# Optimization experiments

Hardware: AMD Instinct MI355X
Metric: run time of the kernel (lower is better)

## Reference

```python
import jax, jax.numpy as jnp
import numpy as np

NUM_NODES = 120000   # entity count
D = 128              # graph_emb_size
T = 10               # time_steps / train_year
B = 64               # batch of input_ids
R = 4                # num_rel
N = 64               # max neighbors per relation (padded)
C = 64               # TCN channel width (output_size)
I = 64               # influence_emb_size
K = 2                # kernel size
L = 8                # TCN levels (num_channels = [64]*8)


def _causal_conv(x, w, b, d):
    # x: [M, Cin, T], w: [Cout, Cin, k] -> causal dilated conv -> [M, Cout, T]
    pad = (w.shape[-1] - 1) * d
    y = jax.lax.conv_general_dilated(x, w, window_strides=(1,), padding=[(pad, 0)],
                                     rhs_dilation=(d,), dimension_numbers=('NCH', 'OIH', 'NCH'))
    return y + b[None, :, None]


def _tcn_last(x, w1_0, b1_0, w2_0, b2_0, down_w, down_b, w1, b1, w2, b2):
    # Bai-style TemporalConvNet; x: [M, D, T] -> last-step state [M, C]
    y = jax.nn.relu(_causal_conv(x, w1_0, b1_0, 1))
    y = jax.nn.relu(_causal_conv(y, w2_0, b2_0, 1))
    h = jax.nn.relu(y + _causal_conv(x, down_w, down_b, 1))  # 1x1 downsample residual (Cin != C)
    for i in range(1, L):
        d = 2 ** i
        y = jax.nn.relu(_causal_conv(h, w1[i - 1], b1[i - 1], d))
        y = jax.nn.relu(_causal_conv(y, w2[i - 1], b2[i - 1], d))
        h = jax.nn.relu(y + h)
    return h[..., -1]


def setup_inputs() -> dict:
    key = jax.random.key(0)
    ks = jax.random.split(key, 16)
    embeddings = jax.random.normal(ks[0], (T, NUM_NODES, D), jnp.float32)
    # entity -> per-year row index; negative = entity absent that year (zero-padded)
    alignment = jax.random.randint(ks[1], (NUM_NODES, T), -NUM_NODES // 5, NUM_NODES).astype(jnp.int32)
    neighbor_idx = jax.random.randint(ks[2], (B, R, N), 0, NUM_NODES).astype(jnp.int32)
    neighbor_mask = jax.random.randint(ks[3], (B, R, N), 0, 2).astype(bool)
    g = lambda k, sh, s: jax.random.normal(k, sh, jnp.float32) * s
    return {
        'embeddings': embeddings,
        'w1_0': g(ks[4], (R, C, D, K), (2.0 / (D * K)) ** 0.5),
        'b1_0': jnp.zeros((R, C), jnp.float32),
        'w2_0': g(ks[5], (R, C, C, K), (2.0 / (C * K)) ** 0.5),
        'b2_0': jnp.zeros((R, C), jnp.float32),
        'down_w': g(ks[6], (R, C, D, 1), (2.0 / D) ** 0.5),
        'down_b': jnp.zeros((R, C), jnp.float32),
        'w1': g(ks[7], (R, L - 1, C, C, K), (2.0 / (C * K)) ** 0.5),
        'b1': jnp.zeros((R, L - 1, C), jnp.float32),
        'w2': g(ks[8], (R, L - 1, C, C, K), (2.0 / (C * K)) ** 0.5),
        'b2': jnp.zeros((R, L - 1, C), jnp.float32),
        'rel_w': g(ks[9], (R, C, I), (2.0 / (C + I)) ** 0.5),
        'alignment': alignment,
        'neighbor_idx': neighbor_idx,
        'neighbor_mask': neighbor_mask,
    }


def reference(embeddings, w1_0, b1_0, w2_0, b2_0, down_w, down_b, w1, b1, w2, b2,
              rel_w, alignment, neighbor_idx, neighbor_mask):
    seq = alignment[neighbor_idx]                                   # [B,R,N,T]
    valid = (seq >= 0) & neighbor_mask[..., None]                   # per-year + existence mask
    idx = jnp.clip(seq, 0)
    # per-year gather: embeddings[t][idx[...,t]] -> [B,R,N,D,T]
    gath = jax.vmap(lambda e, i: e[i], in_axes=(0, -1), out_axes=-1)(embeddings, idx)
    x = gath * valid[:, :, :, None, :].astype(gath.dtype)           # zero-pad absent years
    x = jnp.transpose(x, (1, 0, 2, 3, 4)).reshape(R, B * N, D, T)   # relation-major, neighbors as batch
    last = jax.vmap(_tcn_last)(x, w1_0, b1_0, w2_0, b2_0, down_w, down_b, w1, b1, w2, b2)  # [R,B*N,C]
    infl = jnp.einsum('rmc,rci->rmi', last, rel_w).reshape(R, B, N, I)
    m = jnp.transpose(neighbor_mask, (1, 0, 2)).astype(infl.dtype)  # [R,B,N] drop padded neighbors
    return jnp.einsum('rbni,rbn->bi', infl, m)                      # sum over neighbors and relations
```

## Files before the change

### kernel.cpp

```cpp
#include <hip/hip_runtime.h>
#include <hip/hip_bf16.h>
#include <stdint.h>

constexpr int NUM_NODES = 120000;
constexpr int Tn = 10;
constexpr int Bb = 64, Rr = 4, Nn = 64, Cc = 64, Ii = 64;
constexpr int G = 8;
constexpr int RSTR  = 147456;
constexpr int OFF0  = 0;
constexpr int OFF1  = 16384;
constexpr int OFF2  = 24576;
constexpr int OFFL0 = 32768;

constexpr int OFF_X  = 0;
constexpr int OFF_H0 = 0;
constexpr int OFF_H1 = 6144;
constexpr int OFF_H2 = 10240;
constexpr int OFF_H3 = 12288;
constexpr int OFF_Y  = 20480;
constexpr int ZOFF   = 30720;
constexpr int SMEMB  = 30976;

typedef __attribute__((ext_vector_type(8))) short bf16x8;
typedef __attribute__((ext_vector_type(4))) float f32x4;
typedef __attribute__((ext_vector_type(4))) short s16x4;

__device__ __forceinline__ short f2bf(float f) {
  __hip_bfloat16 h = __float2bfloat16(f);
  return *reinterpret_cast<short*>(&h);
}
__device__ __forceinline__ float bf2f(short s) {
  union { unsigned int u; float f; } x;
  x.u = ((unsigned int)(unsigned short)s) << 16;
  return x.f;
}

extern "C" __global__ void prep_kernel(const float* __restrict__ w1_0,
                                       const float* __restrict__ w2_0,
                                       const float* __restrict__ down_w,
                                       const float* __restrict__ w1s,
                                       const float* __restrict__ w2s,
                                       short* __restrict__ Wf) {
  int i0 = blockIdx.x * blockDim.x + threadIdx.x;
  int stride = gridDim.x * blockDim.x;
  for (int e = i0; e < Rr * RSTR; e += stride) {
    int r = e / RSTR, q = e - r * RSTR;
    float v;
    if (q < 16384) {
      int j = q & 7, lane = (q >> 3) & 63, ks = (q >> 9) & 3, ct = (q >> 11) & 3, tap = (q >> 13) & 1;
      int cout = ct * 16 + (lane & 15), cin = ks * 32 + (lane >> 4) * 8 + j;
      v = w1_0[((r * 64 + cout) * 128 + cin) * 2 + tap];
    } else if (q < 24576) {
      int q2 = q - 16384;
      int j = q2 & 7, lane = (q2 >> 3) & 63, ks = (q2 >> 9) & 3, ct = (q2 >> 11) & 3;
      int cout = ct * 16 + (lane & 15), cin = ks * 32 + (lane >> 4) * 8 + j;
      v = down_w[(r * 64 + cout) * 128 + cin];
    } else if (q < 32768) {
      int q2 = q - 24576;
      int j = q2 & 7, lane = (q2 >> 3) & 63, ks = (q2 >> 9) & 1, ct = (q2 >> 10) & 3, tap = (q2 >> 12) & 1;
      int cout = ct * 16 + (lane & 15), cin = ks * 32 + (lane >> 4) * 8 + j;
      v = w2_0[((r * 64 + cout) * 64 + cin) * 2 + tap];
    } else {
      int q2 = q - 32768;
      int lc = q2 >> 13;
      int l = lc >> 1, jw = lc & 1;
      int q3 = q2 & 8191;
      int j = q3 & 7, lane = (q3 >> 3) & 63, ks = (q3 >> 9) & 1, ct = (q3 >> 10) & 3, tap = (q3 >> 12) & 1;
      int cout = ct * 16 + (lane & 15), cin = ks * 32 + (lane >> 4) * 8 + j;
      const float* src = jw ? w2s : w1s;
      v = src[(((r * 7 + l) * 64 + cout) * 64 + cin) * 2 + tap];
    }
    Wf[e] = f2bf(v);
  }
}

template <int KSN, int NMT, int NTAP, int ROWB>
__device__ __forceinline__ void conv_sp(const char* __restrict__ sm, int srcOff,
                                        const short* __restrict__ wf1,
                                        const short* __restrict__ wf0,
                                        const float* __restrict__ bias,
                                        const int (&T1)[NMT * 2], const int (&T0)[NMT * 2],
                                        int lane, int ct, f32x4 (&acc)[NMT]) {
  const int c16 = (lane >> 4) * 16;
  const int seq = lane & 7;
  const int hi = (lane & 15) >> 3;
  const int sw = seq << 4;
  float bv[4];
#pragma unroll
  for (int g = 0; g < 4; ++g) bv[g] = bias[ct * 16 + (lane >> 4) * 4 + g];
#pragma unroll
  for (int mt = 0; mt < NMT; ++mt) acc[mt] = (f32x4){bv[0], bv[1], bv[2], bv[3]};
  bf16x8 af1[KSN], af0[KSN];
#pragma unroll
  for (int ks = 0; ks < KSN; ++ks)
    af1[ks] = *(const bf16x8*)(wf1 + ((ct * KSN + ks) * 64 + lane) * 8);
  if (NTAP == 2) {
#pragma unroll
    for (int ks = 0; ks < KSN; ++ks)
      af0[ks] = *(const bf16x8*)(wf0 + ((ct * KSN + ks) * 64 + lane) * 8);
  }
#pragma unroll
  for (int mt = 0; mt < NMT; ++mt) {
    int s1 = hi ? T1[2 * mt + 1] : T1[2 * mt];
    const char* p1 = sm + ((s1 < 0) ? ZOFF : srcOff + (s1 * 8 + seq) * ROWB);
#pragma unroll
    for (int ks = 0; ks < KSN; ++ks) {
      bf16x8 b = *(const bf16x8*)(p1 + ((ks * 64 + c16) ^ sw));
      acc[mt] = __builtin_amdgcn_mfma_f32_16x16x32_bf16(af1[ks], b, acc[mt], 0, 0, 0);
    }
    if (NTAP == 2) {
      int s0 = hi ? T0[2 * mt + 1] : T0[2 * mt];
      const char* p0 = sm + ((s0 < 0) ? ZOFF : srcOff + (s0 * 8 + seq) * ROWB);
#pragma unroll
      for (int ks = 0; ks < KSN; ++ks) {
        bf16x8 b = *(const bf16x8*)(p0 + ((ks * 64 + c16) ^ sw));
        acc[mt] = __builtin_amdgcn_mfma_f32_16x16x32_bf16(af0[ks], b, acc[mt], 0, 0, 0);
      }
    }
  }
}

template <int NMT>
__device__ __forceinline__ void store_sp(char* __restrict__ sm, int dstOff, int lane,
                                         int ct, const f32x4 (&v)[NMT]) {
  const int co = ct * 32 + (lane >> 4) * 8;
#pragma unroll
  for (int mt = 0; mt < NMT; ++mt) {
    int oc = 16 * mt + (lane & 15);
    s16x4 p;
#pragma unroll
    for (int g = 0; g < 4; ++g) p[g] = f2bf(v[mt][g]);
    *(s16x4*)(sm + dstOff + oc * 128 + (co ^ ((oc & 7) << 4))) = p;
  }
}

#define RELU_ALL(A, N)                                        \
  _Pragma("unroll") for (int _t = 0; _t < N; ++_t)            \
      _Pragma("unroll") for (int _g = 0; _g < 4; ++_g)        \
          A[_t][_g] = fmaxf(A[_t][_g], 0.f);

template <int NMT>
__device__ __forceinline__ void resid_sp(const char* __restrict__ sm, int prevOff,
                                         const int (&R)[NMT * 2], int lane, int ct,
                                         f32x4 (&a)[NMT]) {
  const int co = ct * 32 + (lane >> 4) * 8;
  const int seq = lane & 7;
  const int hi = (lane & 15) >> 3;
  const int sw = seq << 4;
#pragma unroll
  for (int mt = 0; mt < NMT; ++mt) {
    int rs = hi ? R[2 * mt + 1] : R[2 * mt];
    const char* p = sm + ((rs < 0) ? ZOFF : prevOff + (rs * 8 + seq) * 128);
    s16x4 q = *(const s16x4*)(p + (co ^ sw));
#pragma unroll
    for (int g = 0; g < 4; ++g)
      a[mt][g] = fmaxf(fmaxf(a[mt][g], 0.f) + bf2f(q[g]), 0.f);
  }
}

extern "C" __global__ void __launch_bounds__(256, 4)
tcn_mfma(const float* __restrict__ emb, const int* __restrict__ align_,
         const int* __restrict__ nidx, const int* __restrict__ nmask,
         const float* __restrict__ b1_0, const float* __restrict__ b2_0,
         const float* __restrict__ down_b, const float* __restrict__ b1s,
         const float* __restrict__ b2s, const short* __restrict__ Wf,
         float* __restrict__ P) {
  __shared__ char sm[SMEMB];
  __shared__ int rowid[80];
  __shared__ float mkv[G];
  __shared__ int mapg[G];
  __shared__ int totv;

  const int tid = threadIdx.x;
  const int lane = tid & 63, ct = tid >> 6;
  const int blk = blockIdx.x;
  const int r = blk >> 9;
  const int blkr = blk & 511;
  const int b = blkr >> 3, chunk = blkr & 7;

  if (tid < 64) {
    int n = tid;
    int msk = nmask[(b * Rr + r) * Nn + n];
    unsigned long long bal = __ballot(msk != 0);
    if (tid < G) mapg[tid] = -1;
    if (tid == 0) totv = (int)__popcll(bal);
    int rank = (int)__popcll(bal & ((1ull << n) - 1ull));
    if (msk != 0 && rank >= chunk * G && rank < chunk * G + G)
      mapg[rank - chunk * G] = n;
  }
  if (tid >= 192 && tid < 224) *(uint64_t*)(sm + ZOFF + (tid - 192) * 8) = 0;
  __syncthreads();
  if (chunk * G >= totv) {
    if (tid < 64) P[((r * Bb + b) * 8 + chunk) * 64 + tid] = 0.f;
    return;
  }

  if (tid < 80) {
    int t = tid >> 3, seq = tid & 7;
    int n2 = mapg[seq];
    int s = -1;
    if (n2 >= 0) {
      int ent = nidx[(b * Rr + r) * Nn + n2];
      s = align_[ent * Tn + t];
    }
    rowid[tid] = (n2 >= 0 && s >= 0) ? s : -1;
    if (t == 0) mkv[seq] = (n2 >= 0) ? 1.0f : 0.0f;
  }
  __syncthreads();

#pragma unroll
  for (int it = 0; it < 10; ++it) {
    int idx = tid + it * 256;
    int col = idx >> 5, d4 = idx & 31;
    int row = rowid[col];
    int t = col >> 3;
    s16x4 p = {0, 0, 0, 0};
    if (row >= 0) {
      const float4 v = *(const float4*)(emb + ((size_t)t * NUM_NODES + row) * 128 + d4 * 4);
      p[0] = f2bf(v.x); p[1] = f2bf(v.y); p[2] = f2bf(v.z); p[3] = f2bf(v.w);
    }
    *(s16x4*)(sm + OFF_X + col * 256 + ((d4 * 8) ^ ((col & 7) << 4))) = p;
  }
  __syncthreads();

  const short* wr = Wf + r * RSTR;

  {
    constexpr int T1[10] = {0, 1, 2, 3, 4, 5, 6, 7, 8, 9};
    constexpr int T0[10] = {-1, 0, 1, 2, 3, 4, 5, 6, 7, 8};
    f32x4 a[5];
    conv_sp<4, 5, 2, 256>(sm, OFF_X, wr + OFF0 + 8192, wr + OFF0, b1_0 + r * 64,
                          T1, T0, lane, ct, a);
    RELU_ALL(a, 5)
    store_sp<5>(sm, OFF_Y, lane, ct, a);
  }
  f32x4 accD[3];
  {
    constexpr int TD[6] = {1, 3, 5, 7, 9, 9};
    conv_sp<4, 3, 1, 256>(sm, OFF_X, wr + OFF1, wr + OFF1, down_b + r * 64,
                          TD, TD, lane, ct, accD);
  }
  __syncthreads();
  {
    constexpr int T1[6] = {1, 3, 5, 7, 9, 9};
    constexpr int T0[6] = {0, 2, 4, 6, 8, 8};
    f32x4 a[3];
    conv_sp<2, 3, 2, 128>(sm, OFF_Y, wr + OFF2 + 4096, wr + OFF2, b2_0 + r * 64,
                          T1, T0, lane, ct, a);
#pragma unroll
    for (int mt = 0; mt < 3; ++mt)
#pragma unroll
      for (int g = 0; g < 4; ++g)
        a[mt][g] = fmaxf(fmaxf(a[mt][g], 0.f) + accD[mt][g], 0.f);
    store_sp<3>(sm, OFF_H0, lane, ct, a);
  }
  __syncthreads();
  {
    constexpr int T1[6] = {0, 1, 2, 3, 4, 4};
    constexpr int T0[6] = {-1, 0, 1, 2, 3, 3};
    f32x4 a[3];
    const short* wb = wr + OFFL0;
    conv_sp<2, 3, 2, 128>(sm, OFF_H0, wb + 4096, wb, b1s + (r * 7 + 0) * 64,
                          T1, T0, lane, ct, a);
    RELU_ALL(a, 3)
    store_sp<3>(sm, OFF_Y, lane, ct, a);
  }
  __syncthreads();
  {
    constexpr int T1[4] = {0, 2, 4, 4};
    constexpr int T0[4] = {-1, 1, 3, 3};
    constexpr int R[4] = {0, 2, 4, 4};
    f32x4 a[2];
    const short* wb = wr + OFFL0 + 8192;
    conv_sp<2, 2, 2, 128>(sm, OFF_Y, wb + 4096, wb, b2s + (r * 7 + 0) * 64,
                          T1, T0, lane, ct, a);
    resid_sp<2>(sm, OFF_H0, R, lane, ct, a);
    store_sp<2>(sm, OFF_H1, lane, ct, a);
  }
  __syncthreads();
  {
    constexpr int T1[4] = {0, 1, 2, 2};
    constexpr int T0[4] = {-1, 0, 1, 1};
    f32x4 a[2];
    const short* wb = wr + OFFL0 + 16384;
    conv_sp<2, 2, 2, 128>(sm, OFF_H1, wb + 4096, wb, b1s + (r * 7 + 1) * 64,
                          T1, T0, lane, ct, a);
    RELU_ALL(a, 2)
    store_sp<2>(sm, OFF_Y, lane, ct, a);
  }
  __syncthreads();
  {
    constexpr int T1[2] = {0, 2};
    constexpr int T0[2] = {-1, 1};
    constexpr int R[2] = {0, 2};
    f32x4 a[1];
    const short* wb = wr + OFFL0 + 16384 + 8192;
    conv_sp<2, 1, 2, 128>(sm, OFF_Y, wb + 4096, wb, b2s + (r * 7 + 1) * 64,
                          T1, T0, lane, ct, a);
    resid_sp<1>(sm, OFF_H1, R, lane, ct, a);
    store_sp<1>(sm, OFF_H2, lane, ct, a);
  }
  __syncthreads();
  {
    constexpr int T1[2] = {0, 1};
    constexpr int T0[2] = {-1, 0};
    f32x4 a[1];
    const short* wb = wr + OFFL0 + 32768;
    conv_sp<2, 1, 2, 128>(sm, OFF_H2, wb + 4096, wb, b1s + (r * 7 + 2) * 64,
                          T1, T0, lane, ct, a);
    RELU_ALL(a, 1)
    store_sp<1>(sm, OFF_Y, lane, ct, a);
  }
  __syncthreads();
  {
    constexpr int T1[2] = {1, 1};
    constexpr int T0[2] = {0, 0};
    constexpr int R[2] = {1, 1};
    f32x4 a[1];
    const short* wb = wr + OFFL0 + 32768 + 8192;
    conv_sp<2, 1, 2, 128>(sm, OFF_Y, wb + 4096, wb, b2s + (r * 7 + 2) * 64,
                          T1, T0, lane, ct, a);
    resid_sp<1>(sm, OFF_H2, R, lane, ct, a);
    store_sp<1>(sm, OFF_H3, lane, ct, a);
  }
  __syncthreads();

  f32x4 hfin[1];
#pragma unroll 1
  for (int li = 0; li < 4; ++li) {
    const short* base = wr + OFFL0 + (3 + li) * 16384;
    const int prevOff = OFF_H3 + li * 1024;
    constexpr int TA[2] = {0, 0};
    {
      f32x4 a[1];
      conv_sp<2, 1, 1, 128>(sm, prevOff, base + 4096, base + 4096,
                            b1s + (r * 7 + 3 + li) * 64, TA, TA, lane, ct, a);
      RELU_ALL(a, 1)
      store_sp<1>(sm, OFF_Y, lane, ct, a);
    }
    __syncthreads();
    {
      f32x4 a[1];
      conv_sp<2, 1, 1, 128>(sm, OFF_Y, base + 8192 + 4096, base + 8192 + 4096,
                            b2s + (r * 7 + 3 + li) * 64, TA, TA, lane, ct, a);
      resid_sp<1>(sm, prevOff, TA, lane, ct, a);
      store_sp<1>(sm, prevOff + 1024, lane, ct, a);
      hfin[0] = a[0];
    }
    __syncthreads();
  }

  float mk = ((lane & 15) < 8) ? mkv[lane & 7] : 0.f;
  float s0 = hfin[0][0] * mk, s1 = hfin[0][1] * mk, s2 = hfin[0][2] * mk, s3 = hfin[0][3] * mk;
#pragma unroll
  for (int m2 = 1; m2 <= 4; m2 <<= 1) {
    s0 += __shfl_xor(s0, m2);
    s1 += __shfl_xor(s1, m2);
    s2 += __shfl_xor(s2, m2);
    s3 += __shfl_xor(s3, m2);
  }
  if ((lane & 15) == 0) {
    int base = ((r * Bb + b) * 8 + chunk) * 64 + ct * 16 + (lane >> 4) * 4;
    P[base + 0] = s0;
    P[base + 1] = s1;
    P[base + 2] = s2;
    P[base + 3] = s3;
  }
}

extern "C" __global__ void reduce_kernel(const float* __restrict__ P,
                                         const float* __restrict__ rel_w,
                                         float* __restrict__ out) {
  __shared__ float Sl[Rr * Cc];
  int b = blockIdx.x, i = threadIdx.x;
  for (int idx = i; idx < Rr * Cc; idx += 64) {
    int rr = idx >> 6, cc = idx & 63;
    float s = 0.f;
    for (int p = 0; p < 8; ++p) s += P[((rr * Bb + b) * 8 + p) * 64 + cc];
    Sl[idx] = s;
  }
  __syncthreads();
  float acc = 0.f;
  for (int r = 0; r < Rr; ++r)
#pragma unroll
    for (int cc = 0; cc < 64; ++cc)
      acc += Sl[r * Cc + cc] * rel_w[(r * Cc + cc) * Ii + i];
  out[b * Ii + i] = acc;
}

extern "C" void kernel_launch(void* const* d_in, const int* in_sizes, int n_in,
                              void* d_out, int out_size, void* d_ws, size_t ws_size,
                              hipStream_t stream) {
  const float* emb    = (const float*)d_in[0];
  const float* w1_0   = (const float*)d_in[1];
  const float* b1_0   = (const float*)d_in[2];
  const float* w2_0   = (const float*)d_in[3];
  const float* b2_0   = (const float*)d_in[4];
  const float* down_w = (const float*)d_in[5];
  const float* down_b = (const float*)d_in[6];
  const float* w1s    = (const float*)d_in[7];
  const float* b1s    = (const float*)d_in[8];
  const float* w2s    = (const float*)d_in[9];
  const float* b2s    = (const float*)d_in[10];
  const float* rel_w  = (const float*)d_in[11];
  const int* align_   = (const int*)d_in[12];
  const int* nidx     = (const int*)d_in[13];
  const int* nmask    = (const int*)d_in[14];

  float* P  = (float*)d_ws;
  short* Wf = (short*)((char*)d_ws + 524288);

  prep_kernel<<<768, 256, 0, stream>>>(w1_0, w2_0, down_w, w1s, w2s, Wf);
  tcn_mfma<<<2048, 256, 0, stream>>>(emb, align_, nidx, nmask, b1_0, b2_0, down_b,
                                     b1s, b2s, Wf, P);
  reduce_kernel<<<Bb, Cc, 0, stream>>>(P, rel_w, (float*)d_out);
}
```

Baseline: 61.43 us.

## Process 16 neighbors per block with 512 threads and split time tiles across wave halves

Each block now handles 16 neighbor sequences instead of 8, so one 16-row MFMA tile holds 16 distinct neighbors rather than 8 duplicated across the tile halves. Work is split over 8 waves (two halves by time tile), which halves the grid and the partial-sum count. The final four single-step levels run on one wave looping over all channel tiles with wave-local waits instead of block barriers. Shared memory per block doubles, which may reduce occupancy, and the tail leaves seven waves idle.

```diff
diff --git a/kernel.cpp b/kernel.cpp
--- a/kernel.cpp
+++ b/kernel.cpp
@@ -5,7 +5,6 @@
 constexpr int NUM_NODES = 120000;
 constexpr int Tn = 10;
 constexpr int Bb = 64, Rr = 4, Nn = 64, Cc = 64, Ii = 64;
-constexpr int G = 8;
 constexpr int RSTR  = 147456;
 constexpr int OFF0  = 0;
 constexpr int OFF1  = 16384;
@@ -14,12 +13,12 @@
 
 constexpr int OFF_X  = 0;
 constexpr int OFF_H0 = 0;
-constexpr int OFF_H1 = 6144;
-constexpr int OFF_H2 = 10240;
-constexpr int OFF_H3 = 12288;
-constexpr int OFF_Y  = 20480;
-constexpr int ZOFF   = 30720;
-constexpr int SMEMB  = 30976;
+constexpr int OFF_H1 = 10240;
+constexpr int OFF_H2 = 16384;
+constexpr int OFF_H3 = 20480;
+constexpr int OFF_Y  = 40960;
+constexpr int ZOFF   = 61440;
+constexpr int SMEMB  = 61696;
 
 typedef __attribute__((ext_vector_type(8))) short bf16x8;
 typedef __attribute__((ext_vector_type(4))) float f32x4;
@@ -79,12 +78,11 @@
                                         const short* __restrict__ wf1,
                                         const short* __restrict__ wf0,
                                         const float* __restrict__ bias,
-                                        const int (&T1)[NMT * 2], const int (&T0)[NMT * 2],
+                                        const int (&T1)[NMT], const int (&T0)[NMT],
                                         int lane, int ct, f32x4 (&acc)[NMT]) {
   const int c16 = (lane >> 4) * 16;
-  const int seq = lane & 7;
-  const int hi = (lane & 15) >> 3;
-  const int sw = seq << 4;
+  const int sw = (lane & 7) << 4;
+  const int cm = lane & 15;
   float bv[4];
 #pragma unroll
   for (int g = 0; g < 4; ++g) bv[g] = bias[ct * 16 + (lane >> 4) * 4 + g];
@@ -101,16 +99,16 @@
   }
 #pragma unroll
   for (int mt = 0; mt < NMT; ++mt) {
-    int s1 = hi ? T1[2 * mt + 1] : T1[2 * mt];
-    const char* p1 = sm + ((s1 < 0) ? ZOFF : srcOff + (s1 * 8 + seq) * ROWB);
+    int s1 = T1[mt];
+    const char* p1 = sm + ((s1 < 0) ? ZOFF : srcOff + (s1 * 16 + cm) * ROWB);
 #pragma unroll
     for (int ks = 0; ks < KSN; ++ks) {
       bf16x8 b = *(const bf16x8*)(p1 + ((ks * 64 + c16) ^ sw));
       acc[mt] = __builtin_amdgcn_mfma_f32_16x16x32_bf16(af1[ks], b, acc[mt], 0, 0, 0);
     }
     if (NTAP == 2) {
-      int s0 = hi ? T0[2 * mt + 1] : T0[2 * mt];
-      const char* p0 = sm + ((s0 < 0) ? ZOFF : srcOff + (s0 * 8 + seq) * ROWB);
+      int s0 = T0[mt];
+      const char* p0 = sm + ((s0 < 0) ? ZOFF : srcOff + (s0 * 16 + cm) * ROWB);
 #pragma unroll
       for (int ks = 0; ks < KSN; ++ks) {
         bf16x8 b = *(const bf16x8*)(p0 + ((ks * 64 + c16) ^ sw));
@@ -121,16 +119,17 @@
 }
 
 template <int NMT>
-__device__ __forceinline__ void store_sp(char* __restrict__ sm, int dstOff, int lane,
-                                         int ct, const f32x4 (&v)[NMT]) {
+__device__ __forceinline__ void store_sp(char* __restrict__ sm, int dstOff, int s0,
+                                         int lane, int ct, const f32x4 (&v)[NMT]) {
   const int co = ct * 32 + (lane >> 4) * 8;
+  const int sw = (lane & 7) << 4;
 #pragma unroll
   for (int mt = 0; mt < NMT; ++mt) {
-    int oc = 16 * mt + (lane & 15);
+    int oc = (s0 + mt) * 16 + (lane & 15);
     s16x4 p;
 #pragma unroll
     for (int g = 0; g < 4; ++g) p[g] = f2bf(v[mt][g]);
-    *(s16x4*)(sm + dstOff + oc * 128 + (co ^ ((oc & 7) << 4))) = p;
+    *(s16x4*)(sm + dstOff + oc * 128 + (co ^ sw)) = p;
   }
 }
 
@@ -141,16 +140,14 @@
 
 template <int NMT>
 __device__ __forceinline__ void resid_sp(const char* __restrict__ sm, int prevOff,
-                                         const int (&R)[NMT * 2], int lane, int ct,
+                                         const int (&R)[NMT], int lane, int ct,
                                          f32x4 (&a)[NMT]) {
   const int co = ct * 32 + (lane >> 4) * 8;
-  const int seq = lane & 7;
-  const int hi = (lane & 15) >> 3;
-  const int sw = seq << 4;
+  const int sw = (lane & 7) << 4;
+  const int cm = lane & 15;
 #pragma unroll
   for (int mt = 0; mt < NMT; ++mt) {
-    int rs = hi ? R[2 * mt + 1] : R[2 * mt];
-    const char* p = sm + ((rs < 0) ? ZOFF : prevOff + (rs * 8 + seq) * 128);
+    const char* p = sm + prevOff + (R[mt] * 16 + cm) * 128;
     s16x4 q = *(const s16x4*)(p + (co ^ sw));
 #pragma unroll
     for (int g = 0; g < 4; ++g)
@@ -158,7 +155,7 @@
   }
 }
 
-extern "C" __global__ void __launch_bounds__(256, 4)
+extern "C" __global__ void __launch_bounds__(512, 4)
 tcn_mfma(const float* __restrict__ emb, const int* __restrict__ align_,
          const int* __restrict__ nidx, const int* __restrict__ nmask,
          const float* __restrict__ b1_0, const float* __restrict__ b2_0,
@@ -166,37 +163,37 @@
          const float* __restrict__ b2s, const short* __restrict__ Wf,
          float* __restrict__ P) {
   __shared__ char sm[SMEMB];
-  __shared__ int rowid[80];
-  __shared__ float mkv[G];
-  __shared__ int mapg[G];
+  __shared__ int rowid[160];
+  __shared__ float mkv[16];
+  __shared__ int mapg[16];
   __shared__ int totv;
 
   const int tid = threadIdx.x;
-  const int lane = tid & 63, ct = tid >> 6;
+  const int lane = tid & 63, wave = tid >> 6;
+  const int ct = wave & 3, half = wave >> 2;
   const int blk = blockIdx.x;
-  const int r = blk >> 9;
-  const int blkr = blk & 511;
-  const int b = blkr >> 3, chunk = blkr & 7;
+  const int r = blk >> 8;
+  const int b = (blk >> 2) & 63, chunk = blk & 3;
 
   if (tid < 64) {
     int n = tid;
     int msk = nmask[(b * Rr + r) * Nn + n];
     unsigned long long bal = __ballot(msk != 0);
-    if (tid < G) mapg[tid] = -1;
+    if (tid < 16) mapg[tid] = -1;
     if (tid == 0) totv = (int)__popcll(bal);
     int rank = (int)__popcll(bal & ((1ull << n) - 1ull));
-    if (msk != 0 && rank >= chunk * G && rank < chunk * G + G)
-      mapg[rank - chunk * G] = n;
-  }
-  if (tid >= 192 && tid < 224) *(uint64_t*)(sm + ZOFF + (tid - 192) * 8) = 0;
-  __syncthreads();
-  if (chunk * G >= totv) {
-    if (tid < 64) P[((r * Bb + b) * 8 + chunk) * 64 + tid] = 0.f;
+    if (msk != 0 && rank >= chunk * 16 && rank < chunk * 16 + 16)
+      mapg[rank - chunk * 16] = n;
+  }
+  if (tid >= 448 && tid < 480) *(uint64_t*)(sm + ZOFF + (tid - 448) * 8) = 0;
+  __syncthreads();
+  if (chunk * 16 >= totv) {
+    if (tid < 64) P[((r * Bb + b) * 4 + chunk) * 64 + tid] = 0.f;
     return;
   }
 
-  if (tid < 80) {
-    int t = tid >> 3, seq = tid & 7;
+  if (tid < 160) {
+    int t = tid >> 4, seq = tid & 15;
     int n2 = mapg[seq];
     int s = -1;
     if (n2 >= 0) {
@@ -210,10 +207,10 @@
 
 #pragma unroll
   for (int it = 0; it < 10; ++it) {
-    int idx = tid + it * 256;
+    int idx = tid + it * 512;
     int col = idx >> 5, d4 = idx & 31;
     int row = rowid[col];
-    int t = col >> 3;
+    int t = col >> 4;
     s16x4 p = {0, 0, 0, 0};
     if (row >= 0) {
       const float4 v = *(const float4*)(emb + ((size_t)t * NUM_NODES + row) * 128 + d4 * 4);
@@ -226,145 +223,151 @@
   const short* wr = Wf + r * RSTR;
 
   {
-    constexpr int T1[10] = {0, 1, 2, 3, 4, 5, 6, 7, 8, 9};
-    constexpr int T0[10] = {-1, 0, 1, 2, 3, 4, 5, 6, 7, 8};
+    static constexpr int T1a[5] = {0, 1, 2, 3, 4}, T0a[5] = {-1, 0, 1, 2, 3};
+    static constexpr int T1b[5] = {5, 6, 7, 8, 9}, T0b[5] = {4, 5, 6, 7, 8};
     f32x4 a[5];
     conv_sp<4, 5, 2, 256>(sm, OFF_X, wr + OFF0 + 8192, wr + OFF0, b1_0 + r * 64,
-                          T1, T0, lane, ct, a);
+                          half ? T1b : T1a, half ? T0b : T0a, lane, ct, a);
     RELU_ALL(a, 5)
-    store_sp<5>(sm, OFF_Y, lane, ct, a);
+    store_sp<5>(sm, OFF_Y, half ? 5 : 0, lane, ct, a);
   }
   f32x4 accD[3];
   {
-    constexpr int TD[6] = {1, 3, 5, 7, 9, 9};
+    static constexpr int TDa[3] = {1, 3, 5}, TDb[3] = {5, 7, 9};
     conv_sp<4, 3, 1, 256>(sm, OFF_X, wr + OFF1, wr + OFF1, down_b + r * 64,
-                          TD, TD, lane, ct, accD);
-  }
-  __syncthreads();
-  {
-    constexpr int T1[6] = {1, 3, 5, 7, 9, 9};
-    constexpr int T0[6] = {0, 2, 4, 6, 8, 8};
+                          half ? TDb : TDa, half ? TDb : TDa, lane, ct, accD);
+  }
+  __syncthreads();
+  {
+    static constexpr int T1a[3] = {1, 3, 5}, T0a[3] = {0, 2, 4};
+    static constexpr int T1b[3] = {5, 7, 9}, T0b[3] = {4, 6, 8};
     f32x4 a[3];
     conv_sp<2, 3, 2, 128>(sm, OFF_Y, wr + OFF2 + 4096, wr + OFF2, b2_0 + r * 64,
-                          T1, T0, lane, ct, a);
+                          half ? T1b : T1a, half ? T0b : T0a, lane, ct, a);
 #pragma unroll
     for (int mt = 0; mt < 3; ++mt)
 #pragma unroll
       for (int g = 0; g < 4; ++g)
         a[mt][g] = fmaxf(fmaxf(a[mt][g], 0.f) + accD[mt][g], 0.f);
-    store_sp<3>(sm, OFF_H0, lane, ct, a);
-  }
-  __syncthreads();
-  {
-    constexpr int T1[6] = {0, 1, 2, 3, 4, 4};
-    constexpr int T0[6] = {-1, 0, 1, 2, 3, 3};
+    store_sp<3>(sm, OFF_H0, half ? 2 : 0, lane, ct, a);
+  }
+  __syncthreads();
+  {
+    static constexpr int T1a[3] = {0, 1, 2}, T0a[3] = {-1, 0, 1};
+    static constexpr int T1b[3] = {2, 3, 4}, T0b[3] = {1, 2, 3};
+    const short* wl = wr + OFFL0;
     f32x4 a[3];
-    const short* wb = wr + OFFL0;
-    conv_sp<2, 3, 2, 128>(sm, OFF_H0, wb + 4096, wb, b1s + (r * 7 + 0) * 64,
-                          T1, T0, lane, ct, a);
+    conv_sp<2, 3, 2, 128>(sm, OFF_H0, wl + 4096, wl, b1s + (r * 7 + 0) * 64,
+                          half ? T1b : T1a, half ? T0b : T0a, lane, ct, a);
     RELU_ALL(a, 3)
-    store_sp<3>(sm, OFF_Y, lane, ct, a);
-  }
-  __syncthreads();
-  {
-    constexpr int T1[4] = {0, 2, 4, 4};
-    constexpr int T0[4] = {-1, 1, 3, 3};
-    constexpr int R[4] = {0, 2, 4, 4};
+    store_sp<3>(sm, OFF_Y, half ? 2 : 0, lane, ct, a);
+  }
+  __syncthreads();
+  {
+    static constexpr int T1a[2] = {0, 2}, T0a[2] = {-1, 1}, Ra[2] = {0, 2};
+    static constexpr int T1b[2] = {2, 4}, T0b[2] = {1, 3}, Rb[2] = {2, 4};
+    const short* wl = wr + OFFL0 + 8192;
     f32x4 a[2];
-    const short* wb = wr + OFFL0 + 8192;
-    conv_sp<2, 2, 2, 128>(sm, OFF_Y, wb + 4096, wb, b2s + (r * 7 + 0) * 64,
-                          T1, T0, lane, ct, a);
-    resid_sp<2>(sm, OFF_H0, R, lane, ct, a);
-    store_sp<2>(sm, OFF_H1, lane, ct, a);
-  }
-  __syncthreads();
-  {
-    constexpr int T1[4] = {0, 1, 2, 2};
-    constexpr int T0[4] = {-1, 0, 1, 1};
+    conv_sp<2, 2, 2, 128>(sm, OFF_Y, wl + 4096, wl, b2s + (r * 7 + 0) * 64,
+                          half ? T1b : T1a, half ? T0b : T0a, lane, ct, a);
+    resid_sp<2>(sm, OFF_H0, half ? Rb : Ra, lane, ct, a);
+    store_sp<2>(sm, OFF_H1, half ? 1 : 0, lane, ct, a);
+  }
+  __syncthreads();
+  {
+    static constexpr int T1a[2] = {0, 1}, T0a[2] = {-1, 0};
+    static constexpr int T1b[2] = {1, 2}, T0b[2] = {0, 1};
+    const short* wl = wr + OFFL0 + 16384;
     f32x4 a[2];
-    const short* wb = wr + OFFL0 + 16384;
-    conv_sp<2, 2, 2, 128>(sm, OFF_H1, wb + 4096, wb, b1s + (r * 7 + 1) * 64,
-                          T1, T0, lane, ct, a);
+    conv_sp<2, 2, 2, 128>(sm, OFF_H1, wl + 4096, wl, b1s + (r * 7 + 1) * 64,
+                          half ? T1b : T1a, half ? T0b : T0a, lane, ct, a);
     RELU_ALL(a, 2)
-    store_sp<2>(sm, OFF_Y, lane, ct, a);
-  }
-  __syncthreads();
-  {
-    constexpr int T1[2] = {0, 2};
-    constexpr int T0[2] = {-1, 1};
-    constexpr int R[2] = {0, 2};
+    store_sp<2>(sm, OFF_Y, half ? 1 : 0, lane, ct, a);
+  }
+  __syncthreads();
+  {
+    static constexpr int T1a[1] = {0}, T0a[1] = {-1}, Ra[1] = {0};
+    static constexpr int T1b[1] = {2}, T0b[1] = {1}, Rb[1] = {2};
+    const short* wl = wr + OFFL0 + 16384 + 8192;
     f32x4 a[1];
-    const short* wb = wr + OFFL0 + 16384 + 8192;
-    conv_sp<2, 1, 2, 128>(sm, OFF_Y, wb + 4096, wb, b2s + (r * 7 + 1) * 64,
-                          T1, T0, lane, ct, a);
-    resid_sp<1>(sm, OFF_H1, R, lane, ct, a);
-    store_sp<1>(sm, OFF_H2, lane, ct, a);
-  }
-  __syncthreads();
-  {
-    constexpr int T1[2] = {0, 1};
-    constexpr int T0[2] = {-1, 0};
+    conv_sp<2, 1, 2, 128>(sm, OFF_Y, wl + 4096, wl, b2s + (r * 7 + 1) * 64,
+                          half ? T1b : T1a, half ? T0b : T0a, lane, ct, a);
+    resid_sp<1>(sm, OFF_H1, half ? Rb : Ra, lane, ct, a);
+    store_sp<1>(sm, OFF_H2, half ? 1 : 0, lane, ct, a);
+  }
+  __syncthreads();
+  {
+    static constexpr int T1a[1] = {0}, T0a[1] = {-1};
+    static constexpr int T1b[1] = {1}, T0b[1] = {0};
+    const short* wl = wr + OFFL0 + 32768;
     f32x4 a[1];
-    const short* wb = wr + OFFL0 + 32768;
-    conv_sp<2, 1, 2, 128>(sm, OFF_H2, wb + 4096, wb, b1s + (r * 7 + 2) * 64,
-                          T1, T0, lane, ct, a);
+    conv_sp<2, 1, 2, 128>(sm, OFF_H2, wl + 4096, wl, b1s + (r * 7 + 2) * 64,
+                          half ? T1b : T1a, half ? T0b : T0a, lane, ct, a);
     RELU_ALL(a, 1)
-    store_sp<1>(sm, OFF_Y, lane, ct, a);
-  }
-  __syncthreads();
-  {
-    constexpr int T1[2] = {1, 1};
-    constexpr int T0[2] = {0, 0};
-    constexpr int R[2] = {1, 1};
+    store_sp<1>(sm, OFF_Y, half ? 1 : 0, lane, ct, a);
+  }
+  __syncthreads();
+  {
+    static constexpr int T1c[1] = {1}, T0c[1] = {0}, Rc[1] = {1};
+    const short* wl = wr + OFFL0 + 32768 + 8192;
     f32x4 a[1];
-    const short* wb = wr + OFFL0 + 32768 + 8192;
-    conv_sp<2, 1, 2, 128>(sm, OFF_Y, wb + 4096, wb, b2s + (r * 7 + 2) * 64,
-                          T1, T0, lane, ct, a);
-    resid_sp<1>(sm, OFF_H2, R, lane, ct, a);
-    store_sp<1>(sm, OFF_H3, lane, ct, a);
-  }
-  __syncthreads();
-
-  f32x4 hfin[1];
+    conv_sp<2, 1, 2, 128>(sm, OFF_Y, wl + 4096, wl, b2s + (r * 7 + 2) * 64,
+                          T1c, T0c, lane, ct, a);
+    resid_sp<1>(sm, OFF_H2, Rc, lane, ct, a);
+    store_sp<1>(sm, OFF_H3, 0, lane, ct, a);
+  }
+  __syncthreads();
+
+  if (wave != 0) return;
+
+  f32x4 hfin[4];
+  static constexpr int TA[1] = {0};
 #pragma unroll 1
   for (int li = 0; li < 4; ++li) {
     const short* base = wr + OFFL0 + (3 + li) * 16384;
-    const int prevOff = OFF_H3 + li * 1024;
-    constexpr int TA[2] = {0, 0};
-    {
+    const int prevOff = OFF_H3 + li * 2048;
+#pragma unroll
+    for (int c2 = 0; c2 < 4; ++c2) {
       f32x4 a[1];
       conv_sp<2, 1, 1, 128>(sm, prevOff, base + 4096, base + 4096,
-                            b1s + (r * 7 + 3 + li) * 64, TA, TA, lane, ct, a);
+                            b1s + (r * 7 + 3 + li) * 64, TA, TA, lane, c2, a);
       RELU_ALL(a, 1)
-      store_sp<1>(sm, OFF_Y, lane, ct, a);
-    }
-    __syncthreads();
-    {
+      store_sp<1>(sm, OFF_Y, 0, lane, c2, a);
+    }
+    __builtin_amdgcn_s_waitcnt(0);
+    __builtin_amdgcn_sched_barrier(0);
+#pragma unroll
+    for (int c2 = 0; c2 < 4; ++c2) {
       f32x4 a[1];
       conv_sp<2, 1, 1, 128>(sm, OFF_Y, base + 8192 + 4096, base + 8192 + 4096,
-                            b2s + (r * 7 + 3 + li) * 64, TA, TA, lane, ct, a);
-      resid_sp<1>(sm, prevOff, TA, lane, ct, a);
-      store_sp<1>(sm, prevOff + 1024, lane, ct, a);
-      hfin[0] = a[0];
-    }
-    __syncthreads();
-  }
-
-  float mk = ((lane & 15) < 8) ? mkv[lane & 7] : 0.f;
-  float s0 = hfin[0][0] * mk, s1 = hfin[0][1] * mk, s2 = hfin[0][2] * mk, s3 = hfin[0][3] * mk;
-#pragma unroll
-  for (int m2 = 1; m2 <= 4; m2 <<= 1) {
-    s0 += __shfl_xor(s0, m2);
-    s1 += __shfl_xor(s1, m2);
-    s2 += __shfl_xor(s2, m2);
-    s3 += __shfl_xor(s3, m2);
-  }
-  if ((lane & 15) == 0) {
-    int base = ((r * Bb + b) * 8 + chunk) * 64 + ct * 16 + (lane >> 4) * 4;
-    P[base + 0] = s0;
-    P[base + 1] = s1;
-    P[base + 2] = s2;
-    P[base + 3] = s3;
+                            b2s + (r * 7 + 3 + li) * 64, TA, TA, lane, c2, a);
+      resid_sp<1>(sm, prevOff, TA, lane, c2, a);
+      if (li < 3) store_sp<1>(sm, prevOff + 2048, 0, lane, c2, a);
+      hfin[c2] = a[0];
+    }
+    __builtin_amdgcn_s_waitcnt(0);
+    __builtin_amdgcn_sched_barrier(0);
+  }
+
+  float mk = mkv[lane & 15];
+#pragma unroll
+  for (int c2 = 0; c2 < 4; ++c2) {
+    float s0 = hfin[c2][0] * mk, s1 = hfin[c2][1] * mk;
+    float s2 = hfin[c2][2] * mk, s3 = hfin[c2][3] * mk;
+#pragma unroll
+    for (int m2 = 1; m2 <= 8; m2 <<= 1) {
+      s0 += __shfl_xor(s0, m2);
+      s1 += __shfl_xor(s1, m2);
+      s2 += __shfl_xor(s2, m2);
+      s3 += __shfl_xor(s3, m2);
+    }
+    if ((lane & 15) == 0) {
+      int base = ((r * Bb + b) * 4 + chunk) * 64 + c2 * 16 + (lane >> 4) * 4;
+      P[base + 0] = s0;
+      P[base + 1] = s1;
+      P[base + 2] = s2;
+      P[base + 3] = s3;
+    }
   }
 }
 
@@ -376,7 +379,7 @@
   for (int idx = i; idx < Rr * Cc; idx += 64) {
     int rr = idx >> 6, cc = idx & 63;
     float s = 0.f;
-    for (int p = 0; p < 8; ++p) s += P[((rr * Bb + b) * 8 + p) * 64 + cc];
+    for (int p = 0; p < 4; ++p) s += P[((rr * Bb + b) * 4 + p) * 64 + cc];
     Sl[idx] = s;
   }
   __syncthreads();
@@ -411,7 +414,7 @@
   short* Wf = (short*)((char*)d_ws + 524288);
 
   prep_kernel<<<768, 256, 0, stream>>>(w1_0, w2_0, down_w, w1s, w2s, Wf);
-  tcn_mfma<<<2048, 256, 0, stream>>>(emb, align_, nidx, nmask, b1_0, b2_0, down_b,
+  tcn_mfma<<<1024, 512, 0, stream>>>(emb, align_, nidx, nmask, b1_0, b2_0, down_b,
                                      b1s, b2s, Wf, P);
   reduce_kernel<<<Bb, Cc, 0, stream>>>(P, rel_w, (float*)d_out);
 }
```

Result: slower. 63.00 us (+2.6%).
